# Kernel optimization log

Measured on AMD Instinct MI355X. Metric: run time of the kernel, lower is better.

## Reference

```python
import jax, jax.numpy as jnp
import numpy as np

B, T, D, H, L, FF, SPLIT = 2, 4096, 256, 4 * 0 + 8, 4, 1024, 2048
HD = D // H
EPS = 1e-5


def _layernorm(x, s, b):
    mu = jnp.mean(x, axis=-1, keepdims=True)
    var = jnp.mean(jnp.square(x - mu), axis=-1, keepdims=True)
    return (x - mu) * jax.lax.rsqrt(var + EPS) * s + b


def setup_inputs() -> dict:
    key = jax.random.key(0)
    ks = jax.random.split(key, 10)
    sc = 0.02
    inp = {
        "rows": jax.random.normal(ks[0], (B, T, D), jnp.float32),
        "train_target_embeddings": jax.random.normal(ks[1], (B, SPLIT, D), jnp.float32),
        "Wq": sc * jax.random.normal(ks[2], (L, D, D), jnp.float32),
        "bq": jnp.zeros((L, D), jnp.float32),
        "Wk": sc * jax.random.normal(ks[3], (L, D, D), jnp.float32),
        "bk": jnp.zeros((L, D), jnp.float32),
        "Wv": sc * jax.random.normal(ks[4], (L, D, D), jnp.float32),
        "bv": jnp.zeros((L, D), jnp.float32),
        "Wo": sc * jax.random.normal(ks[5], (L, D, D), jnp.float32),
        "bo": jnp.zeros((L, D), jnp.float32),
        "W1": sc * jax.random.normal(ks[6], (L, D, FF), jnp.float32),
        "b1": jnp.zeros((L, FF), jnp.float32),
        "W2": sc * jax.random.normal(ks[7], (L, FF, D), jnp.float32),
        "b2": jnp.zeros((L, D), jnp.float32),
        "ln1_s": jnp.ones((L, D), jnp.float32),
        "ln1_b": jnp.zeros((L, D), jnp.float32),
        "ln2_s": jnp.ones((L, D), jnp.float32),
        "ln2_b": jnp.zeros((L, D), jnp.float32),
        "split": SPLIT,
    }
    return inp


def reference(rows, train_target_embeddings, Wq, bq, Wk, bk, Wv, bv, Wo, bo,
              W1, b1, W2, b2, ln1_s, ln1_b, ln2_s, ln2_b, split):
    # residual add of train target embeddings onto the train rows
    x = rows.at[:, :split, :].add(train_target_embeddings)
    t = x.shape[1]
    # allowed mask: every query can see all train columns; test queries also see themselves
    key_is_train = jnp.arange(t) < split                      # [T]
    allowed = key_is_train[None, :] | jnp.eye(t, dtype=bool)  # [T,T]
    neg = jnp.asarray(-1e9, x.dtype)
    scale = 1.0 / np.sqrt(HD)
    n_layers = Wq.shape[0]
    for l in range(n_layers):
        # multi-head attention with structured mask
        q = (x @ Wq[l] + bq[l]).reshape(x.shape[0], t, H, HD)
        k = (x @ Wk[l] + bk[l]).reshape(x.shape[0], t, H, HD)
        v = (x @ Wv[l] + bv[l]).reshape(x.shape[0], t, H, HD)
        logits = jnp.einsum('bqhd,bkhd->bhqk', q, k) * scale
        logits = jnp.where(allowed[None, None], logits, neg)
        attn = jax.nn.softmax(logits, axis=-1)
        o = jnp.einsum('bhqk,bkhd->bqhd', attn, v).reshape(x.shape[0], t, D)
        x = _layernorm(x + (o @ Wo[l] + bo[l]), ln1_s[l], ln1_b[l])
        # feed-forward
        h = jax.nn.gelu(x @ W1[l] + b1[l])
        x = _layernorm(x + (h @ W2[l] + b2[l]), ln2_s[l], ln2_b[l])
    return x
```

## Files before the change

### kernel.cpp

```cpp
#include <hip/hip_runtime.h>
#include <cstdint>
#include <cstddef>

#define TSEQ 4096
#define BATCH 2
#define DIM 256
#define NHEAD 8
#define HDIM 32
#define NLAYER 4
#define FFDIM 1024
#define SPLITN 2048
#define MROWS (BATCH * TSEQ)

#define QSCALE 0.2550784545f

typedef __attribute__((ext_vector_type(4))) float f32x4;
typedef __attribute__((ext_vector_type(8))) short bf16x8;

__device__ __forceinline__ short f2bf(float f) {
  union { float f; uint32_t u; } v; v.f = f;
  uint32_t r = v.u + 0x7fffu + ((v.u >> 16) & 1u);
  return (short)(r >> 16);
}

__device__ __forceinline__ float bf2f(short s) {
  union { uint32_t u; float f; } v; v.u = ((uint32_t)(uint16_t)s) << 16;
  return v.f;
}

__device__ __forceinline__ float fast_exp2(float x) {
#if __has_builtin(__builtin_amdgcn_exp2f)
  return __builtin_amdgcn_exp2f(x);
#else
  float r;
  asm volatile("v_exp_f32 %0, %1\n\ts_nop 1" : "=v"(r) : "v"(x));
  return r;
#endif
}

__device__ __forceinline__ uint32_t pack2bf(float a, float b) {
  union { float f; uint32_t u; } ua, ub; ua.f = a; ub.f = b;
  return ((ua.u + 0x8000u) >> 16) | ((ub.u + 0x8000u) & 0xffff0000u);
}

__device__ __forceinline__ float gelu_f(float x) {
  float u = 0.7978845608f * x * (1.0f + 0.044715f * x * x);
  u = fminf(fmaxf(u, -20.f), 20.f);
  float e = fast_exp2(2.885390082f * u);
  float t = (e - 1.0f) / (e + 1.0f);
  return 0.5f * x * (1.0f + t);
}

#define AS1 __attribute__((address_space(1)))
#define AS3 __attribute__((address_space(3)))
__device__ __forceinline__ void gload16(const void* g, void* l) {
  __builtin_amdgcn_global_load_lds((AS1 void*)g, (AS3 void*)l, 16, 0, 0);
}

__global__ __launch_bounds__(256) void prep_w(
    const float* __restrict__ Wq, const float* __restrict__ Wk,
    const float* __restrict__ Wv, const float* __restrict__ Wo,
    const float* __restrict__ W1, const float* __restrict__ W2,
    short* __restrict__ qkvT, short* __restrict__ woT,
    short* __restrict__ w1T, short* __restrict__ w2T)
{
  const int NQKV = NLAYER * 768 * DIM;
  const int NO   = NLAYER * DIM * DIM;
  const int NF   = NLAYER * FFDIM * DIM;
  const int total = NQKV + NO + 2 * NF;
  for (int idx = blockIdx.x * 256 + threadIdx.x; idx < total; idx += gridDim.x * 256) {
    if (idx < NQKV) {
      const int l = idx / (768 * DIM);
      const int rem = idx - l * 768 * DIM;
      const int n = rem >> 8, k = rem & 255;
      const float* src = (n < 256) ? Wq : ((n < 512) ? Wk : Wv);
      qkvT[idx] = f2bf(src[((size_t)l * DIM + k) * DIM + (n & 255)]);
    } else if (idx < NQKV + NO) {
      const int j = idx - NQKV;
      const int l = j >> 16;
      const int rem = j & 65535;
      const int n = rem >> 8, k = rem & 255;
      woT[j] = f2bf(Wo[((size_t)l * DIM + k) * DIM + n]);
    } else if (idx < NQKV + NO + NF) {
      const int j = idx - NQKV - NO;
      const int l = j >> 18;
      const int rem = j & 262143;
      const int n = rem >> 8, k = rem & 255;
      w1T[j] = f2bf(W1[((size_t)l * DIM + k) * FFDIM + n]);
    } else {
      const int j = idx - NQKV - NO - NF;
      const int l = j >> 18;
      const int rem = j & 262143;
      const int n = rem >> 10, k = rem & 1023;
      w2T[j] = f2bf(W2[((size_t)l * FFDIM + k) * DIM + n]);
    }
  }
}

__global__ __launch_bounds__(256) void prep_x(
    const float* __restrict__ rows, const float* __restrict__ tte,
    float* __restrict__ xf, short* __restrict__ xb)
{
  const size_t idx = (size_t)blockIdx.x * 256 + threadIdx.x;
  float4 v = ((const float4*)rows)[idx];
  const size_t e = idx * 4;
  const int m = (int)(e >> 8);
  const int d = (int)(e & 255);
  const int t = m & (TSEQ - 1);
  const int bb = m >> 12;
  if (t < SPLITN) {
    const float4 a = ((const float4*)tte)[((size_t)bb * SPLITN + t) * (DIM / 4) + (d >> 2)];
    v.x += a.x; v.y += a.y; v.z += a.z; v.w += a.w;
  }
  ((float4*)xf)[idx] = v;
  short4 pk; pk.x = f2bf(v.x); pk.y = f2bf(v.y); pk.z = f2bf(v.z); pk.w = f2bf(v.w);
  ((short4*)xb)[idx] = pk;
}

__global__ __launch_bounds__(256, 2) void qkv_gemm(
    const short* __restrict__ A, const short* __restrict__ BT,
    const float* __restrict__ bq, const float* __restrict__ bk,
    const float* __restrict__ bv, short* __restrict__ Cout)
{
  __shared__ short As[128 * 64];
  __shared__ short Bs[128 * 64];
  const int tid = threadIdx.x;
  const int lane = tid & 63;
  const int wave = tid >> 6;
  const int wm = wave & 1, wn = wave >> 1;
  const int col = lane & 15, quad = lane >> 4;

  const short* Ab = A + (size_t)blockIdx.x * 128 * DIM;
  const short* Bb = BT + (size_t)blockIdx.y * 128 * DIM;

  const f32x4 fz = {0.f, 0.f, 0.f, 0.f};
  f32x4 acc[4][4];
#pragma unroll
  for (int i = 0; i < 4; ++i)
#pragma unroll
    for (int j = 0; j < 4; ++j) acc[i][j] = fz;

  for (int k0 = 0; k0 < DIM; k0 += 64) {
#pragma unroll
    for (int p = 0; p < 4; ++p) {
      int i = p * 256 + tid;
      gload16(Ab + (size_t)(i >> 3) * DIM + k0 + (i & 7) * 8, &As[i * 8]);
      gload16(Bb + (size_t)(i >> 3) * DIM + k0 + (i & 7) * 8, &Bs[i * 8]);
    }
    __syncthreads();
#pragma unroll
    for (int ks = 0; ks < 64; ks += 32) {
      bf16x8 af[4], bf[4];
#pragma unroll
      for (int tm = 0; tm < 4; ++tm)
        af[tm] = *(const bf16x8*)&As[(wm * 64 + tm * 16 + col) * 64 + ks + quad * 8];
#pragma unroll
      for (int tn = 0; tn < 4; ++tn)
        bf[tn] = *(const bf16x8*)&Bs[(wn * 64 + tn * 16 + col) * 64 + ks + quad * 8];
#pragma unroll
      for (int tm = 0; tm < 4; ++tm)
#pragma unroll
        for (int tn = 0; tn < 4; ++tn)
          acc[tm][tn] = __builtin_amdgcn_mfma_f32_16x16x32_bf16(af[tm], bf[tn], acc[tm][tn], 0, 0, 0);
    }
    __syncthreads();
  }

#pragma unroll
  for (int tm = 0; tm < 4; ++tm) {
    const int mbase = blockIdx.x * 128 + wm * 64 + tm * 16 + quad * 4;
#pragma unroll
    for (int tn = 0; tn < 4; ++tn) {
      const int n = blockIdx.y * 128 + wn * 64 + tn * 16 + col;
      const float bvv = (n < 256) ? bq[n] : ((n < 512) ? bk[n - 256] : bv[n - 512]);
      const float sc = (n < 256) ? QSCALE : 1.0f;
#pragma unroll
      for (int r = 0; r < 4; ++r)
        Cout[(size_t)(mbase + r) * 768 + n] = f2bf((acc[tm][tn][r] + bvv) * sc);
    }
  }
}

__global__ __launch_bounds__(256, 3) void wo_ln(
    const float* __restrict__ Opart, const float* __restrict__ lpart,
    const short* __restrict__ BT, const float* __restrict__ bias,
    const float* __restrict__ xres,
    const float* __restrict__ gs, const float* __restrict__ gb,
    float* __restrict__ xoutf, short* __restrict__ xoutb)
{
  __shared__ short As[32 * 64];
  __shared__ short Bs[256 * 64];
  __shared__ float ssum[4][32], ssq[4][32];
  const int tid = threadIdx.x;
  const int lane = tid & 63;
  const int wave = tid >> 6;
  const int col = lane & 15, quad = lane >> 4;
  const int m0 = blockIdx.x * 32;

  const f32x4 fz = {0.f, 0.f, 0.f, 0.f};
  f32x4 acc[2][4];
#pragma unroll
  for (int i = 0; i < 2; ++i)
#pragma unroll
    for (int j = 0; j < 4; ++j) acc[i][j] = fz;

  const int arow = tid >> 3;
  const int agr  = tid & 7;
  const int grow = m0 + arow;
  const int tt = grow & (TSEQ - 1), bb = grow >> 12;

  for (int k0 = 0; k0 < DIM; k0 += 64) {
    {
      const int head = (k0 >> 5) + (agr >= 4 ? 1 : 0);
      const size_t lidx = (size_t)(bb * 8 + head) * TSEQ + tt;
      const float l = lpart[lidx] + lpart[(size_t)16 * TSEQ + lidx];
      const float li = 1.0f / l;
      const size_t obase = (size_t)grow * DIM + k0 + agr * 8;
      const float4 a0 = *(const float4*)(Opart + obase);
      const float4 a1 = *(const float4*)(Opart + obase + 4);
      const float4 c0 = *(const float4*)(Opart + (size_t)MROWS * DIM + obase);
      const float4 c1 = *(const float4*)(Opart + (size_t)MROWS * DIM + obase + 4);
      uint4 w;
      w.x = pack2bf((a0.x + c0.x) * li, (a0.y + c0.y) * li);
      w.y = pack2bf((a0.z + c0.z) * li, (a0.w + c0.w) * li);
      w.z = pack2bf((a1.x + c1.x) * li, (a1.y + c1.y) * li);
      w.w = pack2bf((a1.z + c1.z) * li, (a1.w + c1.w) * li);
      *(uint4*)&As[arow * 64 + ((agr ^ (arow & 7)) * 8)] = w;
    }
#pragma unroll
    for (int p = 0; p < 8; ++p) {
      int i = p * 256 + tid;
      gload16(BT + (size_t)(i >> 3) * DIM + k0 + (i & 7) * 8, &Bs[i * 8]);
    }
    __syncthreads();
#pragma unroll
    for (int ks = 0; ks < 64; ks += 32) {
      bf16x8 af[2], bfr[4];
#pragma unroll
      for (int tm = 0; tm < 2; ++tm) {
        const int row = tm * 16 + col;
        const int g = (ks >> 3) + quad;
        af[tm] = *(const bf16x8*)&As[row * 64 + ((g ^ (row & 7)) * 8)];
      }
#pragma unroll
      for (int tn = 0; tn < 4; ++tn)
        bfr[tn] = *(const bf16x8*)&Bs[(wave * 64 + tn * 16 + col) * 64 + ks + quad * 8];
#pragma unroll
      for (int tm = 0; tm < 2; ++tm)
#pragma unroll
        for (int tn = 0; tn < 4; ++tn)
          acc[tm][tn] = __builtin_amdgcn_mfma_f32_16x16x32_bf16(af[tm], bfr[tn], acc[tm][tn], 0, 0, 0);
    }
    __syncthreads();
  }

  const float* resb = xres + (size_t)m0 * DIM;
#pragma unroll
  for (int tn = 0; tn < 4; ++tn) {
    const int n = wave * 64 + tn * 16 + col;
    const float bv = bias[n];
#pragma unroll
    for (int tm = 0; tm < 2; ++tm)
#pragma unroll
      for (int r = 0; r < 4; ++r) {
        const int row = tm * 16 + quad * 4 + r;
        acc[tm][tn][r] += bv + resb[(size_t)row * DIM + n];
      }
  }

#pragma unroll
  for (int tm = 0; tm < 2; ++tm)
#pragma unroll
    for (int r = 0; r < 4; ++r) {
      float s = 0.f, q = 0.f;
#pragma unroll
      for (int tn = 0; tn < 4; ++tn) { const float v = acc[tm][tn][r]; s += v; q += v * v; }
      s += __shfl_xor(s, 1); q += __shfl_xor(q, 1);
      s += __shfl_xor(s, 2); q += __shfl_xor(q, 2);
      s += __shfl_xor(s, 4); q += __shfl_xor(q, 4);
      s += __shfl_xor(s, 8); q += __shfl_xor(q, 8);
      if (col == 0) { const int row = tm * 16 + quad * 4 + r; ssum[wave][row] = s; ssq[wave][row] = q; }
    }
  __syncthreads();
  if (tid < 32) {
    const float S = ssum[0][tid] + ssum[1][tid] + ssum[2][tid] + ssum[3][tid];
    const float Q = ssq[0][tid] + ssq[1][tid] + ssq[2][tid] + ssq[3][tid];
    const float mu = S * (1.0f / DIM);
    const float var = Q * (1.0f / DIM) - mu * mu;
    ssum[0][tid] = mu;
    ssq[0][tid] = rsqrtf(var + 1e-5f);
  }
  __syncthreads();

#pragma unroll
  for (int tm = 0; tm < 2; ++tm)
#pragma unroll
    for (int tn = 0; tn < 4; ++tn) {
      const int n = wave * 64 + tn * 16 + col;
      const float g = gs[n], bb2 = gb[n];
#pragma unroll
      for (int r = 0; r < 4; ++r) {
        const int row = tm * 16 + quad * 4 + r;
        const float out = (acc[tm][tn][r] - ssum[0][row]) * ssq[0][row] * g + bb2;
        xoutf[(size_t)(m0 + row) * DIM + n] = out;
        xoutb[(size_t)(m0 + row) * DIM + n] = f2bf(out);
      }
    }
}

#define HP 1032

__global__ __launch_bounds__(256, 1) void ff_fused(
    const short* __restrict__ xbA, const short* __restrict__ w1T,
    const float* __restrict__ b1, const short* __restrict__ w2T,
    const float* __restrict__ b2, const float* __restrict__ xres,
    const float* __restrict__ gs, const float* __restrict__ gb,
    float* __restrict__ xoutf, short* __restrict__ xoutb)
{
  __shared__ short As[32 * 256];
  __shared__ short Wb[2][64 * 256];
  __shared__ short Hs[32 * HP];
  __shared__ float ssum[4][32], ssq[4][32];

  const int tid = threadIdx.x;
  const int lane = tid & 63;
  const int wave = tid >> 6;
  const int col = lane & 15, quad = lane >> 4;
  const int m0 = blockIdx.x * 32;

#pragma unroll
  for (int p = 0; p < 4; ++p) {
    int i = p * 256 + tid;
    const int row = i >> 5, gp = i & 31;
    gload16(xbA + (size_t)(m0 + row) * DIM + ((gp ^ (row & 7)) * 8), &As[i * 8]);
  }
#pragma unroll
  for (int p = 0; p < 8; ++p) {
    int i = p * 256 + tid;
    const int row = i >> 5, gp = i & 31;
    gload16(w1T + (size_t)row * DIM + ((gp ^ (row & 7)) * 8), &Wb[0][i * 8]);
  }

  const f32x4 fz = {0.f, 0.f, 0.f, 0.f};
  bf16x8 af1[2][8];

  for (int nt = 0; nt < 16; ++nt) {
    __syncthreads();
    if (nt + 1 < 16) {
#pragma unroll
      for (int p = 0; p < 8; ++p) {
        int i = p * 256 + tid;
        const int row = i >> 5, gp = i & 31;
        gload16(w1T + (size_t)((nt + 1) * 64 + row) * DIM + ((gp ^ (row & 7)) * 8),
                &Wb[(nt + 1) & 1][i * 8]);
      }
    }
    if (nt == 0) {
#pragma unroll
      for (int tm = 0; tm < 2; ++tm) {
        const int row = tm * 16 + col;
#pragma unroll
        for (int kf = 0; kf < 8; ++kf)
          af1[tm][kf] = *(const bf16x8*)&As[(row * 32 + ((kf * 4 + quad) ^ (row & 7))) * 8];
      }
    }
    const short* wb = Wb[nt & 1];
    f32x4 a0 = fz, a1 = fz;
    const int brow = wave * 16 + col;
#pragma unroll
    for (int kf = 0; kf < 8; ++kf) {
      const bf16x8 bfv = *(const bf16x8*)&wb[(brow * 32 + ((kf * 4 + quad) ^ (brow & 7))) * 8];
      a0 = __builtin_amdgcn_mfma_f32_16x16x32_bf16(af1[0][kf], bfv, a0, 0, 0, 0);
      a1 = __builtin_amdgcn_mfma_f32_16x16x32_bf16(af1[1][kf], bfv, a1, 0, 0, 0);
    }
    const int n = nt * 64 + wave * 16 + col;
    const float bv = b1[n];
#pragma unroll
    for (int r = 0; r < 4; ++r) {
      Hs[(quad * 4 + r) * HP + n]      = f2bf(gelu_f(a0[r] + bv));
      Hs[(16 + quad * 4 + r) * HP + n] = f2bf(gelu_f(a1[r] + bv));
    }
  }
  __syncthreads();

#pragma unroll
  for (int p = 0; p < 8; ++p) {
    int i = p * 256 + tid;
    const int row = i >> 3, gp = i & 7;
    gload16(w2T + (size_t)row * FFDIM + ((gp ^ (row & 7)) * 8), &Wb[0][i * 8]);
  }

  f32x4 acc[2][4];
#pragma unroll
  for (int i = 0; i < 2; ++i)
#pragma unroll
    for (int j = 0; j < 4; ++j) acc[i][j] = fz;

  for (int kt = 0; kt < 16; ++kt) {
    __syncthreads();
    if (kt + 1 < 16) {
#pragma unroll
      for (int p = 0; p < 8; ++p) {
        int i = p * 256 + tid;
        const int row = i >> 3, gp = i & 7;
        gload16(w2T + (size_t)row * FFDIM + (kt + 1) * 64 + ((gp ^ (row & 7)) * 8),
                &Wb[(kt + 1) & 1][i * 8]);
      }
    }
    const short* wb = Wb[kt & 1];
#pragma unroll
    for (int ks = 0; ks < 2; ++ks) {
      bf16x8 af[2], bfr[4];
#pragma unroll
      for (int tm = 0; tm < 2; ++tm)
        af[tm] = *(const bf16x8*)&Hs[(tm * 16 + col) * HP + kt * 64 + ks * 32 + quad * 8];
#pragma unroll
      for (int tn = 0; tn < 4; ++tn) {
        const int row = wave * 64 + tn * 16 + col;
        bfr[tn] = *(const bf16x8*)&wb[(row * 8 + ((ks * 4 + quad) ^ (row & 7))) * 8];
      }
#pragma unroll
      for (int tm = 0; tm < 2; ++tm)
#pragma unroll
        for (int tn = 0; tn < 4; ++tn)
          acc[tm][tn] = __builtin_amdgcn_mfma_f32_16x16x32_bf16(af[tm], bfr[tn], acc[tm][tn], 0, 0, 0);
    }
  }

  const float* resb = xres + (size_t)m0 * DIM;
#pragma unroll
  for (int tn = 0; tn < 4; ++tn) {
    const int n = wave * 64 + tn * 16 + col;
    const float bv = b2[n];
#pragma unroll
    for (int tm = 0; tm < 2; ++tm)
#pragma unroll
      for (int r = 0; r < 4; ++r) {
        const int row = tm * 16 + quad * 4 + r;
        acc[tm][tn][r] += bv + resb[(size_t)row * DIM + n];
      }
  }
#pragma unroll
  for (int tm = 0; tm < 2; ++tm)
#pragma unroll
    for (int r = 0; r < 4; ++r) {
      float s = 0.f, q = 0.f;
#pragma unroll
      for (int tn = 0; tn < 4; ++tn) { const float v = acc[tm][tn][r]; s += v; q += v * v; }
      s += __shfl_xor(s, 1); q += __shfl_xor(q, 1);
      s += __shfl_xor(s, 2); q += __shfl_xor(q, 2);
      s += __shfl_xor(s, 4); q += __shfl_xor(q, 4);
      s += __shfl_xor(s, 8); q += __shfl_xor(q, 8);
      if (col == 0) { const int row = tm * 16 + quad * 4 + r; ssum[wave][row] = s; ssq[wave][row] = q; }
    }
  __syncthreads();
  if (tid < 32) {
    const float S = ssum[0][tid] + ssum[1][tid] + ssum[2][tid] + ssum[3][tid];
    const float Q = ssq[0][tid] + ssq[1][tid] + ssq[2][tid] + ssq[3][tid];
    const float mu = S * (1.0f / DIM);
    const float var = Q * (1.0f / DIM) - mu * mu;
    ssum[0][tid] = mu;
    ssq[0][tid] = rsqrtf(var + 1e-5f);
  }
  __syncthreads();
#pragma unroll
  for (int tm = 0; tm < 2; ++tm)
#pragma unroll
    for (int tn = 0; tn < 4; ++tn) {
      const int n = wave * 64 + tn * 16 + col;
      const float g = gs[n], bb2 = gb[n];
#pragma unroll
      for (int r = 0; r < 4; ++r) {
        const int row = tm * 16 + quad * 4 + r;
        const float out = (acc[tm][tn][r] - ssum[0][row]) * ssq[0][row] * g + bb2;
        xoutf[(size_t)(m0 + row) * DIM + n] = out;
        xoutb[(size_t)(m0 + row) * DIM + n] = f2bf(out);
      }
    }
}

#define AKT 64
#define KSPL 1024
#define NKT (KSPL / AKT)

__global__ __launch_bounds__(256, 4) void attn_kernel(
    const short* __restrict__ qkv,
    float* __restrict__ Opart, float* __restrict__ lpart)
{
  __shared__ short Kbuf[2][AKT * HDIM];
  __shared__ short Vbuf[2][HDIM * AKT];
  __shared__ short Pall[4][32][72];
  __shared__ float Pdiag[4][16];

  const int tid = threadIdx.x;
  const int lane = tid & 63;
  const int wave = tid >> 6;
  const int col = lane & 15, quad = lane >> 4;
  const int bh = blockIdx.y;
  const int b = bh >> 3, h = bh & 7;
  const int hz = blockIdx.z;
  const int q0 = blockIdx.x * 128 + wave * 32;

  short (*P)[72] = Pall[wave];

  const short* qbase = qkv + (size_t)b * TSEQ * 768 + h * HDIM;
  const short* kbase = qbase + 256;
  const short* vcol  = qbase + 512;

  const short* ksrc = kbase + (size_t)(hz * KSPL + (tid & 63)) * 768 + (tid >> 6) * 8;

  const int vhg = (tid & 127) >> 5, vpr = tid & 31;
  const int vva = vpr >> 2, vb8 = (vpr & 3) * 2;
  const short* vsrc = vcol + (size_t)(hz * KSPL + 2 * vpr) * 768 + vhg * 8;
  const bool vact = (tid < 128);

  const bf16x8 qf0 = *(const bf16x8*)(qbase + (size_t)(q0 + col) * 768 + quad * 8);
  const bf16x8 qf1 = *(const bf16x8*)(qbase + (size_t)(q0 + 16 + col) * 768 + quad * 8);

  bf16x8 ones;
#pragma unroll
  for (int i = 0; i < 8; ++i) ones[i] = (short)0x3F80;

  const f32x4 fz = {0.f, 0.f, 0.f, 0.f};
  f32x4 o[2][2] = {{fz, fz}, {fz, fz}};
  f32x4 lacc[2] = {fz, fz};

  gload16(ksrc, &Kbuf[0][tid * 8]);
  bf16x8 vn0, vn1;
  if (vact) {
    const bf16x8 v0 = *(const bf16x8*)vsrc;
    const bf16x8 v1 = *(const bf16x8*)(vsrc + 768);
#pragma unroll
    for (int j = 0; j < 8; ++j) {
      const uint32_t w = (uint32_t)(uint16_t)v0[j] | ((uint32_t)(uint16_t)v1[j] << 16);
      *(uint32_t*)&Vbuf[0][(vhg * 8 + j) * 64 + ((vva ^ j) * 8) + vb8] = w;
    }
    vn0 = *(const bf16x8*)(vsrc + (size_t)AKT * 768);
    vn1 = *(const bf16x8*)(vsrc + (size_t)AKT * 768 + 768);
  }

  int cur = 0;
  for (int t = 0; t < NKT; ++t) {
    __syncthreads();
    if (t + 1 < NKT) {
      gload16(ksrc + (size_t)(t + 1) * AKT * 768, &Kbuf[1 - cur][tid * 8]);
      if (vact) {
#pragma unroll
        for (int j = 0; j < 8; ++j) {
          const uint32_t w = (uint32_t)(uint16_t)vn0[j] | ((uint32_t)(uint16_t)vn1[j] << 16);
          *(uint32_t*)&Vbuf[1 - cur][(vhg * 8 + j) * 64 + ((vva ^ j) * 8) + vb8] = w;
        }
        if (t + 2 < NKT) {
          vn0 = *(const bf16x8*)(vsrc + (size_t)(t + 2) * AKT * 768);
          vn1 = *(const bf16x8*)(vsrc + (size_t)(t + 2) * AKT * 768 + 768);
        }
      }
    }
    const short* kb = Kbuf[cur];
    const short* vb = Vbuf[cur];

#pragma unroll
    for (int st = 0; st < 4; ++st) {
      const bf16x8 kf = *(const bf16x8*)&kb[(quad * 64 + st * 16 + col) * 8];
      const f32x4 s0 = __builtin_amdgcn_mfma_f32_16x16x32_bf16(kf, qf0, fz, 0, 0, 0);
      const f32x4 s1 = __builtin_amdgcn_mfma_f32_16x16x32_bf16(kf, qf1, fz, 0, 0, 0);
      uint2 w0, w1;
      w0.x = pack2bf(fast_exp2(s0[0]), fast_exp2(s0[1]));
      w0.y = pack2bf(fast_exp2(s0[2]), fast_exp2(s0[3]));
      w1.x = pack2bf(fast_exp2(s1[0]), fast_exp2(s1[1]));
      w1.y = pack2bf(fast_exp2(s1[2]), fast_exp2(s1[3]));
      *(uint2*)&P[col][st * 16 + quad * 4] = w0;
      *(uint2*)&P[16 + col][st * 16 + quad * 4] = w1;
    }
    asm volatile("s_waitcnt lgkmcnt(0)" ::: "memory");

#pragma unroll
    for (int kh = 0; kh < 2; ++kh) {
      const bf16x8 pf0 = *(const bf16x8*)&P[col][kh * 32 + quad * 8];
      const bf16x8 pf1 = *(const bf16x8*)&P[16 + col][kh * 32 + quad * 8];
#pragma unroll
      for (int hh = 0; hh < 2; ++hh) {
        const int hd = hh * 16 + col;
        const bf16x8 vf = *(const bf16x8*)&vb[hd * AKT + (((kh * 4 + quad) ^ (hd & 7)) * 8)];
        o[0][hh] = __builtin_amdgcn_mfma_f32_16x16x32_bf16(pf0, vf, o[0][hh], 0, 0, 0);
        o[1][hh] = __builtin_amdgcn_mfma_f32_16x16x32_bf16(pf1, vf, o[1][hh], 0, 0, 0);
      }
      lacc[0] = __builtin_amdgcn_mfma_f32_16x16x32_bf16(pf0, ones, lacc[0], 0, 0, 0);
      lacc[1] = __builtin_amdgcn_mfma_f32_16x16x32_bf16(pf1, ones, lacc[1], 0, 0, 0);
    }
    cur ^= 1;
  }

  if (hz == 1 && blockIdx.x >= SPLITN / 128) {
#pragma unroll
    for (int qsub = 0; qsub < 2; ++qsub) {
      const int qd = q0 + qsub * 16;
      const bf16x8 qf = qsub ? qf1 : qf0;
      const bf16x8 kf = *(const bf16x8*)(kbase + (size_t)(qd + col) * 768 + quad * 8);
      const f32x4 sd = __builtin_amdgcn_mfma_f32_16x16x32_bf16(kf, qf, fz, 0, 0, 0);
      float ps = 0.f;
#pragma unroll
      for (int r = 0; r < 4; ++r)
        if (quad * 4 + r == col) ps = fast_exp2(sd[r]);
      if (quad == (col >> 2)) Pdiag[wave][col] = ps;
      asm volatile("s_waitcnt lgkmcnt(0)" ::: "memory");
      const f32x4 pv = *(const f32x4*)&Pdiag[wave][quad * 4];
#pragma unroll
      for (int r = 0; r < 4; ++r) {
        lacc[qsub][r] += pv[r];
        const size_t vrow = (size_t)(qd + quad * 4 + r) * 768;
#pragma unroll
        for (int hh = 0; hh < 2; ++hh)
          o[qsub][hh][r] += pv[r] * bf2f(vcol[vrow + hh * 16 + col]);
      }
      asm volatile("s_waitcnt lgkmcnt(0)" ::: "memory");
    }
  }

  float* Ob = Opart + (size_t)hz * MROWS * DIM;
  float* lb = lpart + (size_t)hz * 16 * TSEQ + (size_t)bh * TSEQ;
#pragma unroll
  for (int qsub = 0; qsub < 2; ++qsub) {
    const f32x4 la = lacc[qsub];
    const int qq = q0 + qsub * 16 + quad * 4;
    const int rowb = b * TSEQ + qq;
#pragma unroll
    for (int r = 0; r < 4; ++r) {
      if (col == 0) lb[qq + r] = la[r];
#pragma unroll
      for (int hh = 0; hh < 2; ++hh)
        Ob[(size_t)(rowb + r) * DIM + h * HDIM + hh * 16 + col] = o[qsub][hh][r];
    }
  }
}

extern "C" void kernel_launch(void* const* d_in, const int* in_sizes, int n_in,
                              void* d_out, int out_size, void* d_ws, size_t ws_size,
                              hipStream_t stream)
{
  const float* rows = (const float*)d_in[0];
  const float* tte  = (const float*)d_in[1];
  const float* Wq = (const float*)d_in[2];  const float* bq = (const float*)d_in[3];
  const float* Wk = (const float*)d_in[4];  const float* bk = (const float*)d_in[5];
  const float* Wv = (const float*)d_in[6];  const float* bv = (const float*)d_in[7];
  const float* Wo = (const float*)d_in[8];  const float* bo = (const float*)d_in[9];
  const float* W1 = (const float*)d_in[10]; const float* b1 = (const float*)d_in[11];
  const float* W2 = (const float*)d_in[12]; const float* b2 = (const float*)d_in[13];
  const float* ln1s = (const float*)d_in[14]; const float* ln1b = (const float*)d_in[15];
  const float* ln2s = (const float*)d_in[16]; const float* ln2b = (const float*)d_in[17];

  char* p = (char*)d_ws;
  float* xf   = (float*)p;  p += (size_t)MROWS * DIM * 4;
  short* xb   = (short*)p;  p += (size_t)MROWS * DIM * 2;
  short* qkv  = (short*)p;  p += (size_t)MROWS * 768 * 2;
  float* Opart = (float*)p; p += (size_t)2 * MROWS * DIM * 4;
  float* lpart = (float*)p; p += (size_t)2 * 16 * TSEQ * 4;
  short* qkvT = (short*)p;  p += (size_t)NLAYER * 768 * DIM * 2;
  short* woT  = (short*)p;  p += (size_t)NLAYER * DIM * DIM * 2;
  short* w1T  = (short*)p;  p += (size_t)NLAYER * FFDIM * DIM * 2;
  short* w2T  = (short*)p;  p += (size_t)NLAYER * DIM * FFDIM * 2;

  prep_w<<<2048, 256, 0, stream>>>(Wq, Wk, Wv, Wo, W1, W2, qkvT, woT, w1T, w2T);
  prep_x<<<MROWS * DIM / 4 / 256, 256, 0, stream>>>(rows, tte, xf, xb);

  for (int l = 0; l < NLAYER; ++l) {
    qkv_gemm<<<dim3(MROWS / 128, 6), 256, 0, stream>>>(
        xb, qkvT + (size_t)l * 768 * DIM, bq + l * DIM, bk + l * DIM, bv + l * DIM, qkv);
    attn_kernel<<<dim3(TSEQ / 128, BATCH * NHEAD, 2), 256, 0, stream>>>(qkv, Opart, lpart);
    wo_ln<<<MROWS / 32, 256, 0, stream>>>(
        Opart, lpart, woT + (size_t)l * DIM * DIM, bo + l * DIM, xf,
        ln1s + l * DIM, ln1b + l * DIM, xf, xb);
    float* xo = (l == NLAYER - 1) ? (float*)d_out : xf;
    ff_fused<<<MROWS / 32, 256, 0, stream>>>(
        xb, w1T + (size_t)l * FFDIM * DIM, b1 + l * FFDIM,
        w2T + (size_t)l * DIM * FFDIM, b2 + l * DIM, xf,
        ln2s + l * DIM, ln2b + l * DIM, xo, xb);
  }
}
```

Measured before the change: 525.6 us.

## Interleave FF1 and FF2 chunk-wise in fused feed-forward kernel

The fused feed-forward kernel now computes the first GEMM plus GELU one 64-wide hidden chunk at a time. Each chunk feeds the second GEMM in the next iteration, instead of running two separate serial phases over a full 32x1024 hidden buffer in LDS. The W1 and W2 tiles are double-buffered in separate LDS arrays, and a small double-buffered hidden tile replaces the large padded hidden buffer. Input A fragments are loaded straight from global memory into registers rather than staged through LDS. The aim is to overlap weight loading and the two matmul phases and remove the phase-transition stall. The cost is more loads in flight per iteration and a more complex pipeline.

```diff
diff --git a/kernel.cpp b/kernel.cpp
--- a/kernel.cpp
+++ b/kernel.cpp
@@ -308,8 +308,6 @@
     }
 }
 
-#define HP 1032
-
 __global__ __launch_bounds__(256, 1) void ff_fused(
     const short* __restrict__ xbA, const short* __restrict__ w1T,
     const float* __restrict__ b1, const short* __restrict__ w2T,
@@ -317,9 +315,9 @@
     const float* __restrict__ gs, const float* __restrict__ gb,
     float* __restrict__ xoutf, short* __restrict__ xoutb)
 {
-  __shared__ short As[32 * 256];
-  __shared__ short Wb[2][64 * 256];
-  __shared__ short Hs[32 * HP];
+  __shared__ short Wb1[2][64 * 256];
+  __shared__ short Wb2[2][256 * 64];
+  __shared__ short Hb[2][32][72];
   __shared__ float ssum[4][32], ssq[4][32];
 
   const int tid = threadIdx.x;
@@ -328,96 +326,105 @@
   const int col = lane & 15, quad = lane >> 4;
   const int m0 = blockIdx.x * 32;
 
-#pragma unroll
-  for (int p = 0; p < 4; ++p) {
-    int i = p * 256 + tid;
-    const int row = i >> 5, gp = i & 31;
-    gload16(xbA + (size_t)(m0 + row) * DIM + ((gp ^ (row & 7)) * 8), &As[i * 8]);
-  }
+  const f32x4 fz = {0.f, 0.f, 0.f, 0.f};
+
+  bf16x8 af1[2][8];
+#pragma unroll
+  for (int tm = 0; tm < 2; ++tm) {
+    const int m = tm * 16 + col;
+#pragma unroll
+    for (int kf = 0; kf < 8; ++kf)
+      af1[tm][kf] = *(const bf16x8*)(xbA + (size_t)(m0 + m) * DIM + kf * 32 + quad * 8);
+  }
+
 #pragma unroll
   for (int p = 0; p < 8; ++p) {
     int i = p * 256 + tid;
     const int row = i >> 5, gp = i & 31;
-    gload16(w1T + (size_t)row * DIM + ((gp ^ (row & 7)) * 8), &Wb[0][i * 8]);
-  }
-
-  const f32x4 fz = {0.f, 0.f, 0.f, 0.f};
-  bf16x8 af1[2][8];
-
-  for (int nt = 0; nt < 16; ++nt) {
+    gload16(w1T + (size_t)row * DIM + ((gp ^ (row & 7)) * 8), &Wb1[0][i * 8]);
+  }
+
+  f32x4 acc[2][4];
+#pragma unroll
+  for (int i = 0; i < 2; ++i)
+#pragma unroll
+    for (int j = 0; j < 4; ++j) acc[i][j] = fz;
+
+  for (int c = 0; c < 16; ++c) {
     __syncthreads();
-    if (nt + 1 < 16) {
+    if (c + 1 < 16) {
 #pragma unroll
       for (int p = 0; p < 8; ++p) {
         int i = p * 256 + tid;
         const int row = i >> 5, gp = i & 31;
-        gload16(w1T + (size_t)((nt + 1) * 64 + row) * DIM + ((gp ^ (row & 7)) * 8),
-                &Wb[(nt + 1) & 1][i * 8]);
-      }
-    }
-    if (nt == 0) {
-#pragma unroll
-      for (int tm = 0; tm < 2; ++tm) {
-        const int row = tm * 16 + col;
-#pragma unroll
-        for (int kf = 0; kf < 8; ++kf)
-          af1[tm][kf] = *(const bf16x8*)&As[(row * 32 + ((kf * 4 + quad) ^ (row & 7))) * 8];
-      }
-    }
-    const short* wb = Wb[nt & 1];
-    f32x4 a0 = fz, a1 = fz;
-    const int brow = wave * 16 + col;
-#pragma unroll
-    for (int kf = 0; kf < 8; ++kf) {
-      const bf16x8 bfv = *(const bf16x8*)&wb[(brow * 32 + ((kf * 4 + quad) ^ (brow & 7))) * 8];
-      a0 = __builtin_amdgcn_mfma_f32_16x16x32_bf16(af1[0][kf], bfv, a0, 0, 0, 0);
-      a1 = __builtin_amdgcn_mfma_f32_16x16x32_bf16(af1[1][kf], bfv, a1, 0, 0, 0);
-    }
-    const int n = nt * 64 + wave * 16 + col;
-    const float bv = b1[n];
-#pragma unroll
-    for (int r = 0; r < 4; ++r) {
-      Hs[(quad * 4 + r) * HP + n]      = f2bf(gelu_f(a0[r] + bv));
-      Hs[(16 + quad * 4 + r) * HP + n] = f2bf(gelu_f(a1[r] + bv));
-    }
-  }
+        gload16(w1T + (size_t)((c + 1) * 64 + row) * DIM + ((gp ^ (row & 7)) * 8),
+                &Wb1[(c + 1) & 1][i * 8]);
+      }
+    }
+#pragma unroll
+    for (int p = 0; p < 8; ++p) {
+      int i = p * 256 + tid;
+      const int row = i >> 3, gp = i & 7;
+      gload16(w2T + (size_t)row * FFDIM + c * 64 + ((gp ^ (row & 7)) * 8),
+              &Wb2[c & 1][i * 8]);
+    }
+
+    {
+      const short* wb = Wb1[c & 1];
+      const int brow = wave * 16 + col;
+      f32x4 a0 = fz, a1 = fz;
+#pragma unroll
+      for (int kf = 0; kf < 8; ++kf) {
+        const bf16x8 bfv = *(const bf16x8*)&wb[(brow * 32 + ((kf * 4 + quad) ^ (brow & 7))) * 8];
+        a0 = __builtin_amdgcn_mfma_f32_16x16x32_bf16(af1[0][kf], bfv, a0, 0, 0, 0);
+        a1 = __builtin_amdgcn_mfma_f32_16x16x32_bf16(af1[1][kf], bfv, a1, 0, 0, 0);
+      }
+      const int n = c * 64 + wave * 16 + col;
+      const float bv = b1[n];
+      const int nl = wave * 16 + col;
+#pragma unroll
+      for (int r = 0; r < 4; ++r) {
+        Hb[c & 1][quad * 4 + r][nl]      = f2bf(gelu_f(a0[r] + bv));
+        Hb[c & 1][16 + quad * 4 + r][nl] = f2bf(gelu_f(a1[r] + bv));
+      }
+    }
+
+    if (c > 0) {
+      const int cp = c - 1;
+      const short* wb = Wb2[cp & 1];
+#pragma unroll
+      for (int kh = 0; kh < 2; ++kh) {
+        bf16x8 af[2], bfr[4];
+#pragma unroll
+        for (int tm = 0; tm < 2; ++tm)
+          af[tm] = *(const bf16x8*)&Hb[cp & 1][tm * 16 + col][(kh * 4 + quad) * 8];
+#pragma unroll
+        for (int tn = 0; tn < 4; ++tn) {
+          const int row = wave * 64 + tn * 16 + col;
+          bfr[tn] = *(const bf16x8*)&wb[(row * 8 + ((kh * 4 + quad) ^ (row & 7))) * 8];
+        }
+#pragma unroll
+        for (int tm = 0; tm < 2; ++tm)
+#pragma unroll
+          for (int tn = 0; tn < 4; ++tn)
+            acc[tm][tn] = __builtin_amdgcn_mfma_f32_16x16x32_bf16(af[tm], bfr[tn], acc[tm][tn], 0, 0, 0);
+      }
+    }
+  }
+
   __syncthreads();
-
-#pragma unroll
-  for (int p = 0; p < 8; ++p) {
-    int i = p * 256 + tid;
-    const int row = i >> 3, gp = i & 7;
-    gload16(w2T + (size_t)row * FFDIM + ((gp ^ (row & 7)) * 8), &Wb[0][i * 8]);
-  }
-
-  f32x4 acc[2][4];
-#pragma unroll
-  for (int i = 0; i < 2; ++i)
-#pragma unroll
-    for (int j = 0; j < 4; ++j) acc[i][j] = fz;
-
-  for (int kt = 0; kt < 16; ++kt) {
-    __syncthreads();
-    if (kt + 1 < 16) {
-#pragma unroll
-      for (int p = 0; p < 8; ++p) {
-        int i = p * 256 + tid;
-        const int row = i >> 3, gp = i & 7;
-        gload16(w2T + (size_t)row * FFDIM + (kt + 1) * 64 + ((gp ^ (row & 7)) * 8),
-                &Wb[(kt + 1) & 1][i * 8]);
-      }
-    }
-    const short* wb = Wb[kt & 1];
-#pragma unroll
-    for (int ks = 0; ks < 2; ++ks) {
+  {
+    const short* wb = Wb2[15 & 1];
+#pragma unroll
+    for (int kh = 0; kh < 2; ++kh) {
       bf16x8 af[2], bfr[4];
 #pragma unroll
       for (int tm = 0; tm < 2; ++tm)
-        af[tm] = *(const bf16x8*)&Hs[(tm * 16 + col) * HP + kt * 64 + ks * 32 + quad * 8];
+        af[tm] = *(const bf16x8*)&Hb[1][tm * 16 + col][(kh * 4 + quad) * 8];
 #pragma unroll
       for (int tn = 0; tn < 4; ++tn) {
         const int row = wave * 64 + tn * 16 + col;
-        bfr[tn] = *(const bf16x8*)&wb[(row * 8 + ((ks * 4 + quad) ^ (row & 7))) * 8];
+        bfr[tn] = *(const bf16x8*)&wb[(row * 8 + ((kh * 4 + quad) ^ (row & 7))) * 8];
       }
 #pragma unroll
       for (int tm = 0; tm < 2; ++tm)
```

New measurement: 518.5 us. About the same (-1.4%).
